# Optimization experiments

Measured on AMD Instinct MI355X. Metric: run time of the kernel, lower is better.

The kernel has to match this reference:

```python
import jax, jax.numpy as jnp
import numpy as np

T = 8192
INPUT = 1024
TRACE = 64
CTX = 16
OUT = 1024
EPS = 1e-5  # equinox LayerNorm default


def _linear(key, out_f, in_f):
    k1, k2 = jax.random.split(key)
    lim = 1.0 / np.sqrt(in_f)
    w = jax.random.uniform(k1, (out_f, in_f), minval=-lim, maxval=lim, dtype=jnp.float32)
    b = jax.random.uniform(k2, (out_f,), minval=-lim, maxval=lim, dtype=jnp.float32)
    return w, b


def setup_inputs() -> dict:
    key = jax.random.key(0)
    ks = jax.random.split(key, 8)
    x = jax.random.normal(ks[0], (T, INPUT), dtype=jnp.float32)
    start = jax.random.randint(ks[1], (T,), 0, 2).astype(bool)
    next_done = jax.random.randint(ks[2], (T,), 0, 2).astype(bool)
    state_re = jnp.zeros((1, TRACE, CTX), dtype=jnp.float32)
    state_im = jnp.zeros((1, TRACE, CTX), dtype=jnp.float32)
    pre_w, pre_b = _linear(ks[3], TRACE, INPUT)
    gi_w, gi_b = _linear(ks[4], TRACE, INPUT)
    go_w, go_b = _linear(ks[5], OUT, INPUT)
    skip_w, skip_b = _linear(ks[6], OUT, INPUT)
    mix_w, mix_b = _linear(ks[7], OUT, 2 * TRACE * CTX)
    # ffa.init: deterministic decay rates a and oscillation freqs b
    ffa_a = jnp.linspace(1e-6, 0.5, TRACE, dtype=jnp.float32)
    ffa_b = (2.0 * jnp.pi / jnp.exp(jnp.linspace(jnp.log(1.0), jnp.log(1024.0), CTX))).astype(jnp.float32)
    return dict(x=x, state_re=state_re, state_im=state_im, start=start, next_done=next_done,
                pre_w=pre_w, pre_b=pre_b, gi_w=gi_w, gi_b=gi_b, go_w=go_w, go_b=go_b,
                skip_w=skip_w, skip_b=skip_b, mix_w=mix_w, mix_b=mix_b,
                ffa_a=ffa_a, ffa_b=ffa_b)


def _ffa_apply(ffa_a, ffa_b, gated_x, state0, start):
    """Resettable complex linear recurrence: s_t = gamma * s_{t-1} + x_t, reset at episode starts.
    gamma = exp(-|a| + i b), outer over (trace, context). Parallelized with an associative scan
    over monoid elements (reset_flag, state, elapsed_steps)."""
    Tn, m = gated_x.shape
    c = ffa_b.shape[0]
    ab = jax.lax.complex(
        jnp.broadcast_to(-jnp.abs(ffa_a)[None, :, None], (1, m, c)),
        jnp.broadcast_to(ffa_b[None, None, :], (1, m, c)),
    )  # [1, m, c] complex: log-gamma per unit timestep

    xc = jnp.broadcast_to(gated_x[:, :, None].astype(jnp.complex64), (Tn, m, c))
    # prepend carried-in recurrent state: timestep 0, no reset
    x_e = jnp.concatenate([state0.astype(jnp.complex64), xc], axis=0)          # [T+1, m, c]
    s_e = jnp.concatenate([jnp.zeros((1, 1, 1), bool), start[:, None, None]], axis=0)
    i_e = jnp.concatenate([jnp.zeros((1, 1, 1), jnp.float32),
                           jnp.ones((Tn, 1, 1), jnp.float32)], axis=0)

    def op(a, b):
        s1, x1, i1 = a
        s2, x2, i2 = b
        # zero the carried state across episode boundaries
        x1 = jnp.where(s2, 0.0, x1)
        i1 = jnp.where(s2, 0.0, i1)
        g = jnp.exp(ab * i2.astype(jnp.complex64))  # decay over i2 elapsed steps
        return (jnp.logical_or(s1, s2), x1 * g + x2, i1 + i2)

    _, states, _ = jax.lax.associative_scan(op, (s_e, x_e, i_e), axis=0)
    return states[1:]  # [T, m, c] complex64


def reference(x, state_re, state_im, start, next_done,
              pre_w, pre_b, gi_w, gi_b, go_w, go_b,
              skip_w, skip_b, mix_w, mix_b, ffa_a, ffa_b):
    gate_in = jax.nn.sigmoid(x @ gi_w.T + gi_b)          # [T, trace]
    pre = x @ pre_w.T + pre_b                            # [T, trace]
    gated_x = pre * gate_in

    state0 = jax.lax.complex(state_re, state_im)         # [1, trace, ctx]
    state = _ffa_apply(ffa_a, ffa_b, gated_x, state0, start)  # [T, trace, ctx] complex

    z_in = jnp.concatenate([jnp.real(state), jnp.imag(state)], axis=-1)
    z_in = z_in.reshape(state.shape[0], -1)              # [T, 2*trace*ctx]
    z = z_in @ mix_w.T + mix_b                           # [T, out]

    gate_out = jax.nn.sigmoid(x @ go_w.T + go_b)         # [T, out]
    skip = x @ skip_w.T + skip_b                         # [T, out]

    zg = z * gate_out
    mu = zg.mean(-1, keepdims=True)
    var = ((zg - mu) ** 2).mean(-1, keepdims=True)
    ln = (zg - mu) / jnp.sqrt(var + EPS)                 # LayerNorm, no affine

    out = ln + skip * (1.0 - gate_out)
    final_state = state[-1:]
    return out, final_state


if __name__ == "__main__":
    inp = setup_inputs()
    out, fs = jax.jit(reference)(**inp)
    print(out.shape, out.dtype, fs.shape, fs.dtype)
```

## Files before the change

kernel.cpp:

```cpp
#include <hip/hip_runtime.h>
#include <math.h>

#define T_DIM 8192
#define IN_DIM 1024
#define TRACE 64
#define CTX 16
#define OUT_DIM 1024
#define KMIX 2048

typedef __attribute__((ext_vector_type(8))) short bf16x8;
typedef __attribute__((ext_vector_type(4))) float f32x4;
typedef __attribute__((ext_vector_type(16))) float f32x16;

__device__ __forceinline__ unsigned short f2bf(float f) {
    unsigned int u = __float_as_uint(f);
    u = (u + 0x7FFFu + ((u >> 16) & 1u)) >> 16;
    return (unsigned short)u;
}
__device__ __forceinline__ float bf2f(unsigned short b) {
    return __uint_as_float(((unsigned int)b) << 16);
}

__device__ __forceinline__ void gl2lds16(const void* g, void* l) {
    __builtin_amdgcn_global_load_lds(
        (const __attribute__((address_space(1))) unsigned int*)g,
        (__attribute__((address_space(3))) unsigned int*)l,
        16, 0, 0);
}


__global__ __launch_bounds__(256) void c0_conv(const float* __restrict__ x,
        const float* __restrict__ gw, const float* __restrict__ sw, const float* __restrict__ mw,
        const float* __restrict__ pw, const float* __restrict__ giw,
        const void* __restrict__ startp,
        unsigned short* __restrict__ xb, unsigned short* __restrict__ gob,
        unsigned short* __restrict__ skb, unsigned short* __restrict__ mixb,
        unsigned short* __restrict__ pwb, unsigned short* __restrict__ gwb,
        unsigned char* __restrict__ mask, unsigned long long* __restrict__ mask64)
{
    if (blockIdx.x == 0) {
        __shared__ int nonbool;
        int tid = threadIdx.x;
        if (tid == 0) nonbool = 0;
        __syncthreads();
        const unsigned int* wv = (const unsigned int*)startp;
        #pragma unroll
        for (int p = 0; p < 8; p++) {
            unsigned int a = wv[tid * 8 + p];
            if (a > 1u) nonbool = 1;
        }
        __syncthreads();
        if (nonbool) {
            const unsigned char* s8 = (const unsigned char*)startp;
            for (int i = tid; i < T_DIM; i += 256) mask[i] = (unsigned char)(s8[i] != 0);
        } else {
            const int* s32 = (const int*)startp;
            for (int i = tid; i < T_DIM; i += 256) mask[i] = (unsigned char)(s32[i] != 0);
        }
        __syncthreads();
        if (tid < 128) {
            unsigned long long wv2 = 0ull;
            int base = tid * 64;
            #pragma unroll 8
            for (int b2 = 0; b2 < 64; b2++)
                wv2 |= ((unsigned long long)(mask[base + b2] & 1)) << b2;
            mask64[tid] = wv2;
        }
    }
    const size_t QX = 2097152, QG = 262144, QS = 262144, QM = 524288, QP = 16384, QI = 16384;
    const size_t total = QX + QG + QS + QM + QP + QI;
    for (size_t q = (size_t)blockIdx.x * blockDim.x + threadIdx.x; q < total;
         q += (size_t)gridDim.x * blockDim.x) {
        const float* src; unsigned short* dst; size_t i;
        if (q < QX)                  { src = x;   dst = xb;   i = q; }
        else if (q < QX+QG)          { src = gw;  dst = gob;  i = q - QX; }
        else if (q < QX+QG+QS)       { src = sw;  dst = skb;  i = q - QX - QG; }
        else if (q < QX+QG+QS+QM)    { src = mw;  dst = mixb; i = q - QX - QG - QS; }
        else if (q < QX+QG+QS+QM+QP) { src = pw;  dst = pwb;  i = q - QX - QG - QS - QM; }
        else                         { src = giw; dst = gwb;  i = q - QX - QG - QS - QM - QP; }
        float4 v = *(const float4*)(src + i * 4);
        ushort4 o;
        o.x = f2bf(v.x); o.y = f2bf(v.y); o.z = f2bf(v.z); o.w = f2bf(v.w);
        *(ushort4*)(dst + i * 4) = o;
    }
}

__global__ __launch_bounds__(256) void k1_mfma(const unsigned short* __restrict__ xb,
        const unsigned short* __restrict__ pwb, const unsigned short* __restrict__ gwb,
        const float* __restrict__ pre_b, const float* __restrict__ gi_b,
        float* __restrict__ gxT)
{
    __shared__ __align__(16) unsigned short As[1024];
    __shared__ __align__(16) unsigned short Bs[4096];
    __shared__ float sgE[64][33];

    const int tid = threadIdx.x;
    const int t0 = blockIdx.x * 32;
    const int lane = tid & 63, w = tid >> 6;
    const int quad = lane >> 4, l16 = lane & 15;
    const int r = tid >> 2, s4 = tid & 3;
    const int csw = (s4 - ((r >> 1) & 3)) & 3;

    f32x4 acc[2][2];
    const f32x4 zero4 = {0.f, 0.f, 0.f, 0.f};
    #pragma unroll
    for (int mi = 0; mi < 2; mi++)
        #pragma unroll
        for (int ni = 0; ni < 2; ni++) acc[mi][ni] = zero4;

    const int sfr = (quad + ((l16 >> 1) & 3)) & 3;

    for (int k0 = 0; k0 < IN_DIM; k0 += 32) {
        __syncthreads();
        if (tid < 128) {
            int ra = tid >> 2;
            int ca = ((tid & 3) - ((ra >> 1) & 3)) & 3;
            gl2lds16(xb + (size_t)(t0 + ra) * IN_DIM + k0 + ca * 8, As + tid * 8);
        }
        gl2lds16(pwb + (size_t)r * IN_DIM + k0 + csw * 8, Bs + tid * 8);
        gl2lds16(gwb + (size_t)r * IN_DIM + k0 + csw * 8, Bs + 2048 + tid * 8);
        asm volatile("s_waitcnt vmcnt(0)" ::: "memory");
        __syncthreads();
        bf16x8 af[2], bf[2];
        #pragma unroll
        for (int mi = 0; mi < 2; mi++)
            af[mi] = *(const bf16x8*)&As[(mi * 16 + l16) * 32 + sfr * 8];
        #pragma unroll
        for (int ni = 0; ni < 2; ni++)
            bf[ni] = *(const bf16x8*)&Bs[(w * 32 + ni * 16 + l16) * 32 + sfr * 8];
        #pragma unroll
        for (int mi = 0; mi < 2; mi++)
            #pragma unroll
            for (int ni = 0; ni < 2; ni++)
                acc[mi][ni] = __builtin_amdgcn_mfma_f32_16x16x32_bf16(af[mi], bf[ni], acc[mi][ni], 0, 0, 0);
    }

    if (w >= 2) {
        #pragma unroll
        for (int mi = 0; mi < 2; mi++)
            #pragma unroll
            for (int ni = 0; ni < 2; ni++) {
                int mg = (w - 2) * 32 + ni * 16 + l16;
                float gb = gi_b[mg];
                #pragma unroll
                for (int rr = 0; rr < 4; rr++) {
                    int tl = mi * 16 + quad * 4 + rr;
                    sgE[mg][tl] = 1.f / (1.f + expf(-(acc[mi][ni][rr] + gb)));
                }
            }
    }
    __syncthreads();
    if (w < 2) {
        #pragma unroll
        for (int mi = 0; mi < 2; mi++)
            #pragma unroll
            for (int ni = 0; ni < 2; ni++) {
                int mp = w * 32 + ni * 16 + l16;
                float pb = pre_b[mp];
                float4 o;
                float* po = &o.x;
                #pragma unroll
                for (int rr = 0; rr < 4; rr++) {
                    int tl = mi * 16 + quad * 4 + rr;
                    po[rr] = (acc[mi][ni][rr] + pb) * sgE[mp][tl];
                }
                *(float4*)&gxT[(size_t)mp * T_DIM + t0 + mi * 16 + quad * 4] = o;
            }
    }
}

__global__ __launch_bounds__(128) void k2_scan(const float* __restrict__ gxT,
        const unsigned long long* __restrict__ mask64,
        const float* __restrict__ state_re, const float* __restrict__ state_im,
        const float* __restrict__ ffa_a, const float* __restrict__ ffa_b,
        unsigned short* __restrict__ zinTb, float* __restrict__ fstate)
{
    const int m = blockIdx.x >> 4;
    const int c = blockIdx.x & 15;
    const int j = threadIdx.x;
    __shared__ __align__(16) float gxs[8192 + 128];
    __shared__ float Br[128], Bi[128], Er[128], Ei[128];
    __shared__ unsigned char Rf[128];
    unsigned int* SB = (unsigned int*)gxs;

    const float am = -fabsf(ffa_a[m]);
    const float bc = ffa_b[c];
    const float er = expf(am);
    const float gr = er * cosf(bc);
    const float gi = er * sinf(bc);

    {
        const float4* gx4 = (const float4*)(gxT + (size_t)m * T_DIM);
        #pragma unroll
        for (int it = 0; it < 16; it++) {
            int g = it * 128 + j;
            float4 v = gx4[g];
            int t = g * 4;
            gxs[t     + ( t      >> 6)] = v.x;
            gxs[t + 1 + ((t + 1) >> 6)] = v.y;
            gxs[t + 2 + ((t + 2) >> 6)] = v.z;
            gxs[t + 3 + ((t + 3) >> 6)] = v.w;
        }
    }
    const unsigned long long mw = mask64[j];
    __syncthreads();

    const int lb = j * 65;
    float sre = 0.f, sim = 0.f;
    #pragma unroll 16
    for (int i = 0; i < 64; i++) {
        if ((mw >> i) & 1ull) { sre = 0.f; sim = 0.f; }
        else { float tr_ = sre * gr - sim * gi; sim = sre * gi + sim * gr; sre = tr_; }
        sre += gxs[lb + i];
    }
    Br[j] = sre; Bi[j] = sim; Rf[j] = (mw != 0ull) ? 1 : 0;
    __syncthreads();
    if (j == 0) {
        float e64  = expf(64.f * am);
        float g64r = e64 * cosf(64.f * bc);
        float g64i = e64 * sinf(64.f * bc);
        float pr = state_re[m * CTX + c], pi = state_im[m * CTX + c];
        for (int q = 0; q < 128; q++) {
            Er[q] = pr; Ei[q] = pi;
            if (Rf[q]) { pr = Br[q]; pi = Bi[q]; }
            else {
                float nr = pr * g64r - pi * g64i + Br[q];
                pi       = pr * g64i + pi * g64r + Bi[q];
                pr = nr;
            }
        }
    }
    __syncthreads();
    sre = Er[j]; sim = Ei[j];
    unsigned int ore[32], oim[32];
    #pragma unroll
    for (int i = 0; i < 64; i++) {
        if ((mw >> i) & 1ull) { sre = 0.f; sim = 0.f; }
        else { float tr_ = sre * gr - sim * gi; sim = sre * gi + sim * gr; sre = tr_; }
        sre += gxs[lb + i];
        unsigned short hr = f2bf(sre), hi_ = f2bf(sim);
        if (i & 1) { ore[i >> 1] |= ((unsigned int)hr) << 16; oim[i >> 1] |= ((unsigned int)hi_) << 16; }
        else       { ore[i >> 1]  = hr;                        oim[i >> 1]  = hi_; }
    }
    if (j == 127) {
        int p = m * CTX + c;
        fstate[p]        = sre;
        fstate[1024 + p] = sim;
    }

    unsigned short* zreb = zinTb + (size_t)(m * 32 + c)      * T_DIM;
    unsigned short* zimb = zinTb + (size_t)(m * 32 + 16 + c) * T_DIM;

    __syncthreads();
    #pragma unroll
    for (int q = 0; q < 32; q++) SB[j * 33 + q] = ore[q];
    __syncthreads();
    #pragma unroll
    for (int it = 0; it < 8; it++) {
        int g = (it * 128 + j) * 4;
        int jj = g >> 5, qq = g & 31;
        uint4 v = *(uint4*)&SB[jj * 33 + qq];
        *(uint4*)(zreb + g * 2) = v;
    }
    __syncthreads();
    #pragma unroll
    for (int q = 0; q < 32; q++) SB[j * 33 + q] = oim[q];
    __syncthreads();
    #pragma unroll
    for (int it = 0; it < 8; it++) {
        int g = (it * 128 + j) * 4;
        int jj = g >> 5, qq = g & 31;
        uint4 v = *(uint4*)&SB[jj * 33 + qq];
        *(uint4*)(zimb + g * 2) = v;
    }
}

__global__ __launch_bounds__(256) void t3_tr(const unsigned short* __restrict__ zinTb,
                                             unsigned short* __restrict__ zinb)
{
    __shared__ unsigned short S[64][72];
    const int k0 = blockIdx.x * 64, t0 = blockIdx.y * 64;
    const int tid = threadIdx.x;
    {
        int kr = tid >> 3, tc = (tid & 7) * 8;
        #pragma unroll
        for (int p = 0; p < 2; p++) {
            int k = kr + p * 32;
            ushort4 a = *(const ushort4*)&zinTb[(size_t)(k0 + k) * T_DIM + t0 + tc];
            ushort4 b = *(const ushort4*)&zinTb[(size_t)(k0 + k) * T_DIM + t0 + tc + 4];
            *(ushort4*)&S[k][tc]     = a;
            *(ushort4*)&S[k][tc + 4] = b;
        }
    }
    __syncthreads();
    {
        int tr = tid >> 3, kc = (tid & 7) * 8;
        #pragma unroll
        for (int p = 0; p < 2; p++) {
            int t = tr + p * 32;
            ushort4 o1, o2;
            o1.x = S[kc+0][t]; o1.y = S[kc+1][t]; o1.z = S[kc+2][t]; o1.w = S[kc+3][t];
            o2.x = S[kc+4][t]; o2.y = S[kc+5][t]; o2.z = S[kc+6][t]; o2.w = S[kc+7][t];
            *(ushort4*)&zinb[(size_t)(t0 + t) * KMIX + k0 + kc]     = o1;
            *(ushort4*)&zinb[(size_t)(t0 + t) * KMIX + k0 + kc + 4] = o2;
        }
    }
}

__global__ __launch_bounds__(512, 2) void gA_gemm(
        const unsigned short* __restrict__ xb,   const unsigned short* __restrict__ zinb,
        const unsigned short* __restrict__ gob,  const unsigned short* __restrict__ skb,
        const unsigned short* __restrict__ mixb,
        const float* __restrict__ go_b, const float* __restrict__ skip_b, const float* __restrict__ mix_b,
        unsigned short* __restrict__ zg, unsigned short* __restrict__ sk2)
{
    __shared__ __align__(16) unsigned short L[49152];
    const int tid = threadIdx.x;
    const int b = blockIdx.x;
    const int xcd = b & 7, q = b >> 3;
    const int t0 = (xcd * 4 + (q >> 3)) * 256;
    const int n0 = (q & 7) * 128;

    const int lane = tid & 63, w = tid >> 6;
    const int wm = w >> 1, wn = w & 1;
    const int l31 = lane & 31, h = lane >> 5;
    const int r = tid >> 2;
    const int csw = ((tid & 3) - ((r >> 1) & 3)) & 3;
    const int c8 = csw * 8;
    const int srot = (l31 >> 1) & 3;
    const int dst8 = tid * 8;

    f32x16 accg[2][2], acck[2][2];
    #pragma unroll
    for (int mi = 0; mi < 2; mi++)
        #pragma unroll
        for (int ni = 0; ni < 2; ni++)
            #pragma unroll
            for (int e = 0; e < 16; e++) { accg[mi][ni][e] = 0.f; acck[mi][ni][e] = 0.f; }

    {
        const unsigned short* gA0 = xb  + (size_t)(t0 + r)       * IN_DIM + c8;
        const unsigned short* gA1 = xb  + (size_t)(t0 + 128 + r) * IN_DIM + c8;
        const unsigned short* gB0 = gob + (size_t)(n0 + r)       * IN_DIM + c8;
        const unsigned short* gC0 = skb + (size_t)(n0 + r)       * IN_DIM + c8;

#define STAGE_F(bufi, kof) do {                         \
        unsigned short* _b = &L[(bufi) * 16384];        \
        gl2lds16(gA0 + (kof), _b + dst8);               \
        gl2lds16(gA1 + (kof), _b + 4096 + dst8);        \
        gl2lds16(gB0 + (kof), _b + 8192 + dst8);        \
        gl2lds16(gC0 + (kof), _b + 12288 + dst8);       \
    } while (0)

        STAGE_F(0, 0);
        STAGE_F(1, 32);
        asm volatile("s_waitcnt vmcnt(4)" ::: "memory");
        __builtin_amdgcn_s_barrier();

        int cur = 0, nx2 = 2;
        for (int t = 0; t < 32; ++t) {
            const unsigned short* As = &L[cur * 16384];
            const unsigned short* Bs = As + 8192;
            const unsigned short* Cs = As + 12288;
            const bool st = (t + 2 < 32);
            #pragma unroll
            for (int kh = 0; kh < 2; kh++) {
                const int so = ((kh * 2 + h + srot) & 3) * 8;
                bf16x8 af[2], bg[2], bk[2];
                #pragma unroll
                for (int mi = 0; mi < 2; mi++)
                    af[mi] = *(const bf16x8*)&As[(wm * 64 + mi * 32 + l31) * 32 + so];
                #pragma unroll
                for (int ni = 0; ni < 2; ni++) {
                    bg[ni] = *(const bf16x8*)&Bs[(wn * 64 + ni * 32 + l31) * 32 + so];
                    bk[ni] = *(const bf16x8*)&Cs[(wn * 64 + ni * 32 + l31) * 32 + so];
                }
                if (kh == 0 && st) STAGE_F(nx2, (t + 2) * 32);
                __builtin_amdgcn_s_setprio(1);
                #pragma unroll
                for (int mi = 0; mi < 2; mi++)
                    #pragma unroll
                    for (int ni = 0; ni < 2; ni++) {
                        accg[mi][ni] = __builtin_amdgcn_mfma_f32_32x32x16_bf16(af[mi], bg[ni], accg[mi][ni], 0, 0, 0);
                        acck[mi][ni] = __builtin_amdgcn_mfma_f32_32x32x16_bf16(af[mi], bk[ni], acck[mi][ni], 0, 0, 0);
                    }
                __builtin_amdgcn_s_setprio(0);
            }
            if (st) { asm volatile("s_waitcnt vmcnt(4)" ::: "memory"); }
            else    { asm volatile("s_waitcnt vmcnt(0)" ::: "memory"); }
            __builtin_amdgcn_s_barrier();
            cur = (cur == 2) ? 0 : cur + 1;
            nx2 = (nx2 == 2) ? 0 : nx2 + 1;
        }
#undef STAGE_F
    }

    unsigned int sigp[32];
    #pragma unroll
    for (int mi = 0; mi < 2; mi++)
        #pragma unroll
        for (int ni = 0; ni < 2; ni++) {
            int n = n0 + wn * 64 + ni * 32 + l31;
            float gb = go_b[n];
            float sb_ = skip_b[n];
            #pragma unroll
            for (int reg = 0; reg < 16; reg++) {
                int row = (reg & 3) + 8 * (reg >> 2) + 4 * h;
                int t = t0 + wm * 64 + mi * 32 + row;
                float s = 1.f / (1.f + expf(-(accg[mi][ni][reg] + gb)));
                sk2[(size_t)t * OUT_DIM + n] = f2bf((acck[mi][ni][reg] + sb_) * (1.f - s));
                unsigned int pk = (unsigned int)f2bf(s);
                int idx = (mi * 2 + ni) * 8 + (reg >> 1);
                if (reg & 1) sigp[idx] |= pk << 16;
                else         sigp[idx]  = pk;
            }
        }

    #pragma unroll
    for (int mi = 0; mi < 2; mi++)
        #pragma unroll
        for (int ni = 0; ni < 2; ni++)
            #pragma unroll
            for (int e = 0; e < 16; e++) accg[mi][ni][e] = 0.f;
    {
        const unsigned short* mA0 = zinb + (size_t)(t0 + r)       * KMIX + c8;
        const unsigned short* mA1 = zinb + (size_t)(t0 + 128 + r) * KMIX + c8;
        const unsigned short* mB0 = mixb + (size_t)(n0 + r)       * KMIX + c8;

#define STAGE_M(bufi, kof) do {                         \
        unsigned short* _b = &L[(bufi) * 16384];        \
        gl2lds16(mA0 + (kof), _b + dst8);               \
        gl2lds16(mA1 + (kof), _b + 4096 + dst8);        \
        gl2lds16(mB0 + (kof), _b + 8192 + dst8);        \
    } while (0)

        STAGE_M(0, 0);
        STAGE_M(1, 32);
        asm volatile("s_waitcnt vmcnt(3)" ::: "memory");
        __builtin_amdgcn_s_barrier();

        int cur = 0, nx2 = 2;
        for (int t = 0; t < 64; ++t) {
            const unsigned short* As = &L[cur * 16384];
            const unsigned short* Bs = As + 8192;
            const bool st = (t + 2 < 64);
            #pragma unroll
            for (int kh = 0; kh < 2; kh++) {
                const int so = ((kh * 2 + h + srot) & 3) * 8;
                bf16x8 af[2], bf[2];
                #pragma unroll
                for (int mi = 0; mi < 2; mi++)
                    af[mi] = *(const bf16x8*)&As[(wm * 64 + mi * 32 + l31) * 32 + so];
                #pragma unroll
                for (int ni = 0; ni < 2; ni++)
                    bf[ni] = *(const bf16x8*)&Bs[(wn * 64 + ni * 32 + l31) * 32 + so];
                if (kh == 0 && st) STAGE_M(nx2, (t + 2) * 32);
                __builtin_amdgcn_s_setprio(1);
                #pragma unroll
                for (int mi = 0; mi < 2; mi++)
                    #pragma unroll
                    for (int ni = 0; ni < 2; ni++)
                        accg[mi][ni] = __builtin_amdgcn_mfma_f32_32x32x16_bf16(af[mi], bf[ni], accg[mi][ni], 0, 0, 0);
                __builtin_amdgcn_s_setprio(0);
            }
            if (st) { asm volatile("s_waitcnt vmcnt(3)" ::: "memory"); }
            else    { asm volatile("s_waitcnt vmcnt(0)" ::: "memory"); }
            __builtin_amdgcn_s_barrier();
            cur = (cur == 2) ? 0 : cur + 1;
            nx2 = (nx2 == 2) ? 0 : nx2 + 1;
        }
#undef STAGE_M
    }

    #pragma unroll
    for (int mi = 0; mi < 2; mi++)
        #pragma unroll
        for (int ni = 0; ni < 2; ni++) {
            int n = n0 + wn * 64 + ni * 32 + l31;
            float mb_ = mix_b[n];
            #pragma unroll
            for (int reg = 0; reg < 16; reg++) {
                int row = (reg & 3) + 8 * (reg >> 2) + 4 * h;
                int t = t0 + wm * 64 + mi * 32 + row;
                unsigned int u = sigp[(mi * 2 + ni) * 8 + (reg >> 1)];
                float sig = bf2f((unsigned short)((reg & 1) ? (u >> 16) : (u & 0xffff)));
                zg[(size_t)t * OUT_DIM + n] = f2bf((accg[mi][ni][reg] + mb_) * sig);
            }
        }
}

__global__ __launch_bounds__(256) void g3_ln(const unsigned short* __restrict__ zg,
        const unsigned short* __restrict__ sk2, const float* __restrict__ fstate,
        float* __restrict__ out, int out_size)
{
    __shared__ float sb[4], qb[4];
    __shared__ float mu_s, rstd_s;
    const int t = blockIdx.x;
    const int tid = threadIdx.x;
    ushort4 zu = *(const ushort4*)&zg [(size_t)t * OUT_DIM + tid * 4];
    ushort4 su = *(const ushort4*)&sk2[(size_t)t * OUT_DIM + tid * 4];
    float z0 = bf2f(zu.x), z1 = bf2f(zu.y), z2 = bf2f(zu.z), z3 = bf2f(zu.w);
    float s0 = bf2f(su.x), s1 = bf2f(su.y), s2 = bf2f(su.z), s3 = bf2f(su.w);
    float s = z0 + z1 + z2 + z3;
    float q = z0*z0 + z1*z1 + z2*z2 + z3*z3;
    #pragma unroll
    for (int off = 32; off > 0; off >>= 1) {
        s += __shfl_down(s, off, 64);
        q += __shfl_down(q, off, 64);
    }
    int wid = tid >> 6;
    if ((tid & 63) == 0) { sb[wid] = s; qb[wid] = q; }
    __syncthreads();
    if (tid == 0) {
        float S = sb[0] + sb[1] + sb[2] + sb[3];
        float Q = qb[0] + qb[1] + qb[2] + qb[3];
        float mu = S * (1.f / 1024.f);
        float var = Q * (1.f / 1024.f) - mu * mu;
        mu_s = mu; rstd_s = rsqrtf(var + 1e-5f);
    }
    __syncthreads();
    float mu = mu_s, rs = rstd_s;
    float4 o;
    o.x = (z0 - mu) * rs + s0;
    o.y = (z1 - mu) * rs + s1;
    o.z = (z2 - mu) * rs + s2;
    o.w = (z3 - mu) * rs + s3;
    *(float4*)&out[(size_t)t * OUT_DIM + tid * 4] = o;

    if (t < 8) {
        int i = t * 256 + tid;
        long long base = (long long)T_DIM * OUT_DIM;
        if (base + i < (long long)out_size) out[base + i] = fstate[i];
    }
}

extern "C" void kernel_launch(void* const* d_in, const int* in_sizes, int n_in,
                              void* d_out, int out_size, void* d_ws, size_t ws_size,
                              hipStream_t stream) {
    const float* x        = (const float*)d_in[0];
    const float* state_re = (const float*)d_in[1];
    const float* state_im = (const float*)d_in[2];
    const void*  startp   = d_in[3];
    const float* pre_w    = (const float*)d_in[5];
    const float* pre_b    = (const float*)d_in[6];
    const float* gi_w     = (const float*)d_in[7];
    const float* gi_b     = (const float*)d_in[8];
    const float* go_w     = (const float*)d_in[9];
    const float* go_b     = (const float*)d_in[10];
    const float* skip_w   = (const float*)d_in[11];
    const float* skip_b   = (const float*)d_in[12];
    const float* mix_w    = (const float*)d_in[13];
    const float* mix_b    = (const float*)d_in[14];
    const float* ffa_a    = (const float*)d_in[15];
    const float* ffa_b    = (const float*)d_in[16];

    float* ws = (float*)d_ws;
    float*          gxT    = ws;
    unsigned short* zinTb  = (unsigned short*)(ws + 524288);
    unsigned short* zinb   = (unsigned short*)(ws + 8912896);
    unsigned short* xb     = (unsigned short*)(ws + 17301504);
    unsigned short* gob    = (unsigned short*)(ws + 21495808);
    unsigned short* skb    = (unsigned short*)(ws + 22020096);
    unsigned short* mixb   = (unsigned short*)(ws + 22544384);
    unsigned short* zg     = (unsigned short*)(ws + 23592960);
    unsigned short* sk2    = (unsigned short*)(ws + 27787264);
    float*          fstate = ws + 31981568;
    unsigned char*  mask   = (unsigned char*)(ws + 31983616);
    unsigned long long* mask64 = (unsigned long long*)(ws + 31985664);
    unsigned short* pwb    = zg;
    unsigned short* gwb    = zg + 65536;
    float* out = (float*)d_out;

    hipLaunchKernelGGL(c0_conv,  dim3(1536),    dim3(256),  0, stream, x, go_w, skip_w, mix_w, pre_w, gi_w,
                                                             startp, xb, gob, skb, mixb, pwb, gwb, mask, mask64);
    hipLaunchKernelGGL(k1_mfma,  dim3(256),     dim3(256),  0, stream, xb, pwb, gwb, pre_b, gi_b, gxT);
    hipLaunchKernelGGL(k2_scan,  dim3(1024),    dim3(128),  0, stream, gxT, mask64, state_re, state_im, ffa_a, ffa_b, zinTb, fstate);
    hipLaunchKernelGGL(t3_tr,    dim3(32, 128), dim3(256),  0, stream, zinTb, zinb);
    hipLaunchKernelGGL(gA_gemm,  dim3(256),     dim3(512),  0, stream, xb, zinb, gob, skb, mixb, go_b, skip_b, mix_b, zg, sk2);
    hipLaunchKernelGGL(g3_ln,    dim3(8192),    dim3(256),  0, stream, zg, sk2, fstate, out, out_size);
}
```

Measured before the change: 271.2 us.

## Fuse scan output transpose into scan via interleaved mix layout; unroll GEMM pipelines

The scan kernel now runs one block per trace row with 1024 threads covering all 16 context columns. It writes real/imag bf16 pairs directly in time-major order, which removes the separate transpose kernel and its intermediate buffer. To match the new interleaved K ordering (re,im adjacent per context), the mix weight conversion permutes columns when casting to bf16. Separately, the triple-buffered GEMM main loops are manually unrolled by three with constant buffer indices and waitcnts. The trade-off is that the scan now uses only 64 blocks and issues strided 4-byte global stores, which may underutilize the GPU and coalesce poorly.

```diff
diff --git a/kernel.cpp b/kernel.cpp
--- a/kernel.cpp
+++ b/kernel.cpp
@@ -67,21 +67,37 @@
             mask64[tid] = wv2;
         }
     }
-    const size_t QX = 2097152, QG = 262144, QS = 262144, QM = 524288, QP = 16384, QI = 16384;
-    const size_t total = QX + QG + QS + QM + QP + QI;
-    for (size_t q = (size_t)blockIdx.x * blockDim.x + threadIdx.x; q < total;
+    const size_t QX = 2097152, QG = 262144, QS = 262144, QP = 16384, QI = 16384;
+    const size_t totalA = QX + QG + QS + QP + QI;
+    for (size_t q = (size_t)blockIdx.x * blockDim.x + threadIdx.x; q < totalA;
          q += (size_t)gridDim.x * blockDim.x) {
         const float* src; unsigned short* dst; size_t i;
-        if (q < QX)                  { src = x;   dst = xb;   i = q; }
-        else if (q < QX+QG)          { src = gw;  dst = gob;  i = q - QX; }
-        else if (q < QX+QG+QS)       { src = sw;  dst = skb;  i = q - QX - QG; }
-        else if (q < QX+QG+QS+QM)    { src = mw;  dst = mixb; i = q - QX - QG - QS; }
-        else if (q < QX+QG+QS+QM+QP) { src = pw;  dst = pwb;  i = q - QX - QG - QS - QM; }
-        else                         { src = giw; dst = gwb;  i = q - QX - QG - QS - QM - QP; }
+        if (q < QX)               { src = x;   dst = xb;   i = q; }
+        else if (q < QX+QG)       { src = gw;  dst = gob;  i = q - QX; }
+        else if (q < QX+QG+QS)    { src = sw;  dst = skb;  i = q - QX - QG; }
+        else if (q < QX+QG+QS+QP) { src = pw;  dst = pwb;  i = q - QX - QG - QS; }
+        else                      { src = giw; dst = gwb;  i = q - QX - QG - QS - QP; }
         float4 v = *(const float4*)(src + i * 4);
         ushort4 o;
         o.x = f2bf(v.x); o.y = f2bf(v.y); o.z = f2bf(v.z); o.w = f2bf(v.w);
         *(ushort4*)(dst + i * 4) = o;
+    }
+    const size_t QM = 524288;
+    for (size_t q = (size_t)blockIdx.x * blockDim.x + threadIdx.x; q < QM;
+         q += (size_t)gridDim.x * blockDim.x) {
+        float4 v = *(const float4*)(mw + q * 4);
+        int flat = (int)(q * 4);
+        int n  = flat >> 11;
+        int kk = flat & 2047;
+        int mm = kk >> 5;
+        int w_ = kk & 31;
+        int p  = w_ >> 4;
+        int cc = w_ & 15;
+        int kb = (n << 11) + mm * 32 + (cc << 1) + p;
+        mixb[kb]     = f2bf(v.x);
+        mixb[kb + 2] = f2bf(v.y);
+        mixb[kb + 4] = f2bf(v.z);
+        mixb[kb + 6] = f2bf(v.w);
     }
 }
 
@@ -169,19 +185,18 @@
     }
 }
 
-__global__ __launch_bounds__(128) void k2_scan(const float* __restrict__ gxT,
+__global__ __launch_bounds__(1024, 1) void k2_scan(const float* __restrict__ gxT,
         const unsigned long long* __restrict__ mask64,
         const float* __restrict__ state_re, const float* __restrict__ state_im,
         const float* __restrict__ ffa_a, const float* __restrict__ ffa_b,
-        unsigned short* __restrict__ zinTb, float* __restrict__ fstate)
+        unsigned short* __restrict__ zinb, float* __restrict__ fstate)
 {
-    const int m = blockIdx.x >> 4;
-    const int c = blockIdx.x & 15;
-    const int j = threadIdx.x;
+    const int m = blockIdx.x;
+    const int tid = threadIdx.x;
+    const int c = tid & 15, j = tid >> 4;
     __shared__ __align__(16) float gxs[8192 + 128];
-    __shared__ float Br[128], Bi[128], Er[128], Ei[128];
-    __shared__ unsigned char Rf[128];
-    unsigned int* SB = (unsigned int*)gxs;
+    __shared__ float Br[16][65], Bi[16][65], Er[16][65], Ei[16][65];
+    __shared__ unsigned char Rf[16][65];
 
     const float am = -fabsf(ffa_a[m]);
     const float bc = ffa_b[c];
@@ -192,8 +207,8 @@
     {
         const float4* gx4 = (const float4*)(gxT + (size_t)m * T_DIM);
         #pragma unroll
-        for (int it = 0; it < 16; it++) {
-            int g = it * 128 + j;
+        for (int it = 0; it < 2; it++) {
+            int g = it * 1024 + tid;
             float4 v = gx4[g];
             int t = g * 4;
             gxs[t     + ( t      >> 6)] = v.x;
@@ -202,108 +217,71 @@
             gxs[t + 3 + ((t + 3) >> 6)] = v.w;
         }
     }
-    const unsigned long long mw = mask64[j];
+    const unsigned long long mw0 = mask64[j * 2];
+    const unsigned long long mw1 = mask64[j * 2 + 1];
     __syncthreads();
 
-    const int lb = j * 65;
+    const int lb = j * 130;
     float sre = 0.f, sim = 0.f;
-    #pragma unroll 16
+    #pragma unroll 8
     for (int i = 0; i < 64; i++) {
-        if ((mw >> i) & 1ull) { sre = 0.f; sim = 0.f; }
+        if ((mw0 >> i) & 1ull) { sre = 0.f; sim = 0.f; }
         else { float tr_ = sre * gr - sim * gi; sim = sre * gi + sim * gr; sre = tr_; }
         sre += gxs[lb + i];
     }
-    Br[j] = sre; Bi[j] = sim; Rf[j] = (mw != 0ull) ? 1 : 0;
+    #pragma unroll 8
+    for (int i = 0; i < 64; i++) {
+        if ((mw1 >> i) & 1ull) { sre = 0.f; sim = 0.f; }
+        else { float tr_ = sre * gr - sim * gi; sim = sre * gi + sim * gr; sre = tr_; }
+        sre += gxs[lb + 65 + i];
+    }
+    Br[c][j] = sre; Bi[c][j] = sim; Rf[c][j] = ((mw0 | mw1) != 0ull) ? 1 : 0;
     __syncthreads();
-    if (j == 0) {
-        float e64  = expf(64.f * am);
-        float g64r = e64 * cosf(64.f * bc);
-        float g64i = e64 * sinf(64.f * bc);
-        float pr = state_re[m * CTX + c], pi = state_im[m * CTX + c];
-        for (int q = 0; q < 128; q++) {
-            Er[q] = pr; Ei[q] = pi;
-            if (Rf[q]) { pr = Br[q]; pi = Bi[q]; }
+
+    if (tid < 16) {
+        const int cc = tid;
+        float b2 = 128.f * ffa_b[cc];
+        float e128 = expf(128.f * am);
+        float gRr = e128 * cosf(b2);
+        float gRi = e128 * sinf(b2);
+        float pr = state_re[m * CTX + cc], pi = state_im[m * CTX + cc];
+        for (int q2 = 0; q2 < 64; q2++) {
+            Er[cc][q2] = pr; Ei[cc][q2] = pi;
+            if (Rf[cc][q2]) { pr = Br[cc][q2]; pi = Bi[cc][q2]; }
             else {
-                float nr = pr * g64r - pi * g64i + Br[q];
-                pi       = pr * g64i + pi * g64r + Bi[q];
+                float nr = pr * gRr - pi * gRi + Br[cc][q2];
+                pi       = pr * gRi + pi * gRr + Bi[cc][q2];
                 pr = nr;
             }
         }
     }
     __syncthreads();
-    sre = Er[j]; sim = Ei[j];
-    unsigned int ore[32], oim[32];
-    #pragma unroll
-    for (int i = 0; i < 64; i++) {
-        if ((mw >> i) & 1ull) { sre = 0.f; sim = 0.f; }
-        else { float tr_ = sre * gr - sim * gi; sim = sre * gi + sim * gr; sre = tr_; }
-        sre += gxs[lb + i];
-        unsigned short hr = f2bf(sre), hi_ = f2bf(sim);
-        if (i & 1) { ore[i >> 1] |= ((unsigned int)hr) << 16; oim[i >> 1] |= ((unsigned int)hi_) << 16; }
-        else       { ore[i >> 1]  = hr;                        oim[i >> 1]  = hi_; }
-    }
-    if (j == 127) {
-        int p = m * CTX + c;
-        fstate[p]        = sre;
-        fstate[1024 + p] = sim;
-    }
-
-    unsigned short* zreb = zinTb + (size_t)(m * 32 + c)      * T_DIM;
-    unsigned short* zimb = zinTb + (size_t)(m * 32 + 16 + c) * T_DIM;
-
-    __syncthreads();
-    #pragma unroll
-    for (int q = 0; q < 32; q++) SB[j * 33 + q] = ore[q];
-    __syncthreads();
-    #pragma unroll
-    for (int it = 0; it < 8; it++) {
-        int g = (it * 128 + j) * 4;
-        int jj = g >> 5, qq = g & 31;
-        uint4 v = *(uint4*)&SB[jj * 33 + qq];
-        *(uint4*)(zreb + g * 2) = v;
-    }
-    __syncthreads();
-    #pragma unroll
-    for (int q = 0; q < 32; q++) SB[j * 33 + q] = oim[q];
-    __syncthreads();
-    #pragma unroll
-    for (int it = 0; it < 8; it++) {
-        int g = (it * 128 + j) * 4;
-        int jj = g >> 5, qq = g & 31;
-        uint4 v = *(uint4*)&SB[jj * 33 + qq];
-        *(uint4*)(zimb + g * 2) = v;
-    }
-}
-
-__global__ __launch_bounds__(256) void t3_tr(const unsigned short* __restrict__ zinTb,
-                                             unsigned short* __restrict__ zinb)
-{
-    __shared__ unsigned short S[64][72];
-    const int k0 = blockIdx.x * 64, t0 = blockIdx.y * 64;
-    const int tid = threadIdx.x;
+
+    sre = Er[c][j]; sim = Ei[c][j];
+    unsigned int* zout = (unsigned int*)zinb;
+    const int obase = m * CTX + c;
     {
-        int kr = tid >> 3, tc = (tid & 7) * 8;
-        #pragma unroll
-        for (int p = 0; p < 2; p++) {
-            int k = kr + p * 32;
-            ushort4 a = *(const ushort4*)&zinTb[(size_t)(k0 + k) * T_DIM + t0 + tc];
-            ushort4 b = *(const ushort4*)&zinTb[(size_t)(k0 + k) * T_DIM + t0 + tc + 4];
-            *(ushort4*)&S[k][tc]     = a;
-            *(ushort4*)&S[k][tc + 4] = b;
-        }
-    }
-    __syncthreads();
-    {
-        int tr = tid >> 3, kc = (tid & 7) * 8;
-        #pragma unroll
-        for (int p = 0; p < 2; p++) {
-            int t = tr + p * 32;
-            ushort4 o1, o2;
-            o1.x = S[kc+0][t]; o1.y = S[kc+1][t]; o1.z = S[kc+2][t]; o1.w = S[kc+3][t];
-            o2.x = S[kc+4][t]; o2.y = S[kc+5][t]; o2.z = S[kc+6][t]; o2.w = S[kc+7][t];
-            *(ushort4*)&zinb[(size_t)(t0 + t) * KMIX + k0 + kc]     = o1;
-            *(ushort4*)&zinb[(size_t)(t0 + t) * KMIX + k0 + kc + 4] = o2;
-        }
+        const int tbase = j * 128;
+        #pragma unroll 8
+        for (int i = 0; i < 64; i++) {
+            if ((mw0 >> i) & 1ull) { sre = 0.f; sim = 0.f; }
+            else { float tr_ = sre * gr - sim * gi; sim = sre * gi + sim * gr; sre = tr_; }
+            sre += gxs[lb + i];
+            unsigned int u = (unsigned int)f2bf(sre) | ((unsigned int)f2bf(sim) << 16);
+            zout[((size_t)(tbase + i) << 10) + obase] = u;
+        }
+        #pragma unroll 8
+        for (int i = 0; i < 64; i++) {
+            if ((mw1 >> i) & 1ull) { sre = 0.f; sim = 0.f; }
+            else { float tr_ = sre * gr - sim * gi; sim = sre * gi + sim * gr; sre = tr_; }
+            sre += gxs[lb + 65 + i];
+            unsigned int u = (unsigned int)f2bf(sre) | ((unsigned int)f2bf(sim) << 16);
+            zout[((size_t)(tbase + 64 + i) << 10) + obase] = u;
+        }
+    }
+    if (j == 63) {
+        fstate[obase]        = sre;
+        fstate[1024 + obase] = sim;
     }
 }
 
@@ -352,46 +330,50 @@
         gl2lds16(gC0 + (kof), _b + 12288 + dst8);       \
     } while (0)
 
+#define STEP_F(T, CUR, NXT, DOST, VMC) do {             \
+        const unsigned short* As = &L[(CUR) * 16384];   \
+        const unsigned short* Bs = As + 8192;           \
+        const unsigned short* Cs = As + 12288;          \
+        _Pragma("unroll")                               \
+        for (int kh = 0; kh < 2; kh++) {                \
+            const int so = ((kh * 2 + h + srot) & 3) * 8; \
+            bf16x8 af[2], bg[2], bk[2];                 \
+            _Pragma("unroll")                           \
+            for (int mi = 0; mi < 2; mi++)              \
+                af[mi] = *(const bf16x8*)&As[(wm * 64 + mi * 32 + l31) * 32 + so]; \
+            _Pragma("unroll")                           \
+            for (int ni = 0; ni < 2; ni++) {            \
+                bg[ni] = *(const bf16x8*)&Bs[(wn * 64 + ni * 32 + l31) * 32 + so]; \
+                bk[ni] = *(const bf16x8*)&Cs[(wn * 64 + ni * 32 + l31) * 32 + so]; \
+            }                                           \
+            if (kh == 0 && (DOST)) STAGE_F(NXT, ((T) + 2) * 32); \
+            __builtin_amdgcn_s_setprio(1);              \
+            _Pragma("unroll")                           \
+            for (int mi = 0; mi < 2; mi++)              \
+                _Pragma("unroll")                       \
+                for (int ni = 0; ni < 2; ni++) {        \
+                    accg[mi][ni] = __builtin_amdgcn_mfma_f32_32x32x16_bf16(af[mi], bg[ni], accg[mi][ni], 0, 0, 0); \
+                    acck[mi][ni] = __builtin_amdgcn_mfma_f32_32x32x16_bf16(af[mi], bk[ni], acck[mi][ni], 0, 0, 0); \
+                }                                       \
+            __builtin_amdgcn_s_setprio(0);              \
+        }                                               \
+        asm volatile("s_waitcnt vmcnt(" #VMC ")" ::: "memory"); \
+        __builtin_amdgcn_s_barrier();                   \
+    } while (0)
+
         STAGE_F(0, 0);
         STAGE_F(1, 32);
         asm volatile("s_waitcnt vmcnt(4)" ::: "memory");
         __builtin_amdgcn_s_barrier();
 
-        int cur = 0, nx2 = 2;
-        for (int t = 0; t < 32; ++t) {
-            const unsigned short* As = &L[cur * 16384];
-            const unsigned short* Bs = As + 8192;
-            const unsigned short* Cs = As + 12288;
-            const bool st = (t + 2 < 32);
-            #pragma unroll
-            for (int kh = 0; kh < 2; kh++) {
-                const int so = ((kh * 2 + h + srot) & 3) * 8;
-                bf16x8 af[2], bg[2], bk[2];
-                #pragma unroll
-                for (int mi = 0; mi < 2; mi++)
-                    af[mi] = *(const bf16x8*)&As[(wm * 64 + mi * 32 + l31) * 32 + so];
-                #pragma unroll
-                for (int ni = 0; ni < 2; ni++) {
-                    bg[ni] = *(const bf16x8*)&Bs[(wn * 64 + ni * 32 + l31) * 32 + so];
-                    bk[ni] = *(const bf16x8*)&Cs[(wn * 64 + ni * 32 + l31) * 32 + so];
-                }
-                if (kh == 0 && st) STAGE_F(nx2, (t + 2) * 32);
-                __builtin_amdgcn_s_setprio(1);
-                #pragma unroll
-                for (int mi = 0; mi < 2; mi++)
-                    #pragma unroll
-                    for (int ni = 0; ni < 2; ni++) {
-                        accg[mi][ni] = __builtin_amdgcn_mfma_f32_32x32x16_bf16(af[mi], bg[ni], accg[mi][ni], 0, 0, 0);
-                        acck[mi][ni] = __builtin_amdgcn_mfma_f32_32x32x16_bf16(af[mi], bk[ni], acck[mi][ni], 0, 0, 0);
-                    }
-                __builtin_amdgcn_s_setprio(0);
-            }
-            if (st) { asm volatile("s_waitcnt vmcnt(4)" ::: "memory"); }
-            else    { asm volatile("s_waitcnt vmcnt(0)" ::: "memory"); }
-            __builtin_amdgcn_s_barrier();
-            cur = (cur == 2) ? 0 : cur + 1;
-            nx2 = (nx2 == 2) ? 0 : nx2 + 1;
-        }
+        for (int t3i = 0; t3i < 30; t3i += 3) {
+            STEP_F(t3i,     0, 2, 1, 4);
+            STEP_F(t3i + 1, 1, 0, 1, 4);
+            STEP_F(t3i + 2, 2, 1, 1, 4);
+        }
+        STEP_F(30, 0, 2, 0, 0);
+        STEP_F(31, 1, 0, 0, 0);
+#undef STEP_F
 #undef STAGE_F
     }
 
@@ -434,41 +416,47 @@
         gl2lds16(mB0 + (kof), _b + 8192 + dst8);        \
     } while (0)
 
+#define STEP_M(T, CUR, NXT, DOST, VMC) do {             \
+        const unsigned short* As = &L[(CUR) * 16384];   \
+        const unsigned short* Bs = As + 8192;           \
+        _Pragma("unroll")                               \
+        for (int kh = 0; kh < 2; kh++) {                \
+            const int so = ((kh * 2 + h + srot) & 3) * 8; \
+            bf16x8 af[2], bf[2];                        \
+            _Pragma("unroll")                           \
+            for (int mi = 0; mi < 2; mi++)              \
+                af[mi] = *(const bf16x8*)&As[(wm * 64 + mi * 32 + l31) * 32 + so]; \
+            _Pragma("unroll")                           \
+            for (int ni = 0; ni < 2; ni++)              \
+                bf[ni] = *(const bf16x8*)&Bs[(wn * 64 + ni * 32 + l31) * 32 + so]; \
+            if (kh == 0 && (DOST)) STAGE_M(NXT, ((T) + 2) * 32); \
+            __builtin_amdgcn_s_setprio(1);              \
+            _Pragma("unroll")                           \
+            for (int mi = 0; mi < 2; mi++)              \
+                _Pragma("unroll")                       \
+                for (int ni = 0; ni < 2; ni++)          \
+                    accg[mi][ni] = __builtin_amdgcn_mfma_f32_32x32x16_bf16(af[mi], bf[ni], accg[mi][ni], 0, 0, 0); \
+            __builtin_amdgcn_s_setprio(0);              \
+        }                                               \
+        asm volatile("s_waitcnt vmcnt(" #VMC ")" ::: "memory"); \
+        __builtin_amdgcn_s_barrier();                   \
+    } while (0)
+
         STAGE_M(0, 0);
         STAGE_M(1, 32);
         asm volatile("s_waitcnt vmcnt(3)" ::: "memory");
         __builtin_amdgcn_s_barrier();
 
-        int cur = 0, nx2 = 2;
-        for (int t = 0; t < 64; ++t) {
-            const unsigned short* As = &L[cur * 16384];
-            const unsigned short* Bs = As + 8192;
-            const bool st = (t + 2 < 64);
-            #pragma unroll
-            for (int kh = 0; kh < 2; kh++) {
-                const int so = ((kh * 2 + h + srot) & 3) * 8;
-                bf16x8 af[2], bf[2];
-                #pragma unroll
-                for (int mi = 0; mi < 2; mi++)
-                    af[mi] = *(const bf16x8*)&As[(wm * 64 + mi * 32 + l31) * 32 + so];
-                #pragma unroll
-                for (int ni = 0; ni < 2; ni++)
-                    bf[ni] = *(const bf16x8*)&Bs[(wn * 64 + ni * 32 + l31) * 32 + so];
-                if (kh == 0 && st) STAGE_M(nx2, (t + 2) * 32);
-                __builtin_amdgcn_s_setprio(1);
-                #pragma unroll
-                for (int mi = 0; mi < 2; mi++)
-                    #pragma unroll
-                    for (int ni = 0; ni < 2; ni++)
-                        accg[mi][ni] = __builtin_amdgcn_mfma_f32_32x32x16_bf16(af[mi], bf[ni], accg[mi][ni], 0, 0, 0);
-                __builtin_amdgcn_s_setprio(0);
-            }
-            if (st) { asm volatile("s_waitcnt vmcnt(3)" ::: "memory"); }
-            else    { asm volatile("s_waitcnt vmcnt(0)" ::: "memory"); }
-            __builtin_amdgcn_s_barrier();
-            cur = (cur == 2) ? 0 : cur + 1;
-            nx2 = (nx2 == 2) ? 0 : nx2 + 1;
-        }
+        for (int t3i = 0; t3i < 60; t3i += 3) {
+            STEP_M(t3i,     0, 2, 1, 3);
+            STEP_M(t3i + 1, 1, 0, 1, 3);
+            STEP_M(t3i + 2, 2, 1, 1, 3);
+        }
+        STEP_M(60, 0, 2, 1, 3);
+        STEP_M(61, 1, 0, 1, 3);
+        STEP_M(62, 2, 1, 0, 0);
+        STEP_M(63, 0, 2, 0, 0);
+#undef STEP_M
 #undef STAGE_M
     }
 
@@ -556,7 +544,6 @@
 
     float* ws = (float*)d_ws;
     float*          gxT    = ws;
-    unsigned short* zinTb  = (unsigned short*)(ws + 524288);
     unsigned short* zinb   = (unsigned short*)(ws + 8912896);
     unsigned short* xb     = (unsigned short*)(ws + 17301504);
     unsigned short* gob    = (unsigned short*)(ws + 21495808);
@@ -571,11 +558,10 @@
     unsigned short* gwb    = zg + 65536;
     float* out = (float*)d_out;
 
-    hipLaunchKernelGGL(c0_conv,  dim3(1536),    dim3(256),  0, stream, x, go_w, skip_w, mix_w, pre_w, gi_w,
-                                                             startp, xb, gob, skb, mixb, pwb, gwb, mask, mask64);
-    hipLaunchKernelGGL(k1_mfma,  dim3(256),     dim3(256),  0, stream, xb, pwb, gwb, pre_b, gi_b, gxT);
-    hipLaunchKernelGGL(k2_scan,  dim3(1024),    dim3(128),  0, stream, gxT, mask64, state_re, state_im, ffa_a, ffa_b, zinTb, fstate);
-    hipLaunchKernelGGL(t3_tr,    dim3(32, 128), dim3(256),  0, stream, zinTb, zinb);
-    hipLaunchKernelGGL(gA_gemm,  dim3(256),     dim3(512),  0, stream, xb, zinb, gob, skb, mixb, go_b, skip_b, mix_b, zg, sk2);
-    hipLaunchKernelGGL(g3_ln,    dim3(8192),    dim3(256),  0, stream, zg, sk2, fstate, out, out_size);
-}
+    hipLaunchKernelGGL(c0_conv,  dim3(1536), dim3(256),  0, stream, x, go_w, skip_w, mix_w, pre_w, gi_w,
+                                                          startp, xb, gob, skb, mixb, pwb, gwb, mask, mask64);
+    hipLaunchKernelGGL(k1_mfma,  dim3(256),  dim3(256),  0, stream, xb, pwb, gwb, pre_b, gi_b, gxT);
+    hipLaunchKernelGGL(k2_scan,  dim3(64),   dim3(1024), 0, stream, gxT, mask64, state_re, state_im, ffa_a, ffa_b, zinb, fstate);
+    hipLaunchKernelGGL(gA_gemm,  dim3(256),  dim3(512),  0, stream, xb, zinb, gob, skb, mixb, go_b, skip_b, mix_b, zg, sk2);
+    hipLaunchKernelGGL(g3_ln,    dim3(8192), dim3(256),  0, stream, zg, sk2, fstate, out, out_size);
+}
```

Measured after the change: 263.4 us. -2.9%, faster.
